# Kernel tuning notes

Measured on AMD Instinct MI355X. Metric: run time of the kernel, lower is better.

## Reference

```python
import jax, jax.numpy as jnp
import numpy as np

EPS_NORM = 1e-12


def _sage_layer(h, src, dst, n_dst, W_self, W_neigh, b):
    # DGL SAGEConv(mean) on a bipartite block: dst nodes = first n_dst src nodes.
    h_dst = h[:n_dst]
    msgs = h[src]                                              # [E, d] irregular gather
    s = jax.ops.segment_sum(msgs, dst, num_segments=n_dst)    # [n_dst, d]
    cnt = jax.ops.segment_sum(jnp.ones((src.shape[0],), h.dtype), dst, num_segments=n_dst)
    agg = s / jnp.maximum(cnt, 1.0)[:, None]                   # mean over in-neighbors (0-deg -> 0)
    out = h_dst @ W_self + agg @ W_neigh + b
    out = jax.nn.relu(out)                                     # activation=F.relu
    nrm = jnp.maximum(jnp.linalg.norm(out, axis=1, keepdims=True), EPS_NORM)
    return out / nrm                                           # norm=F.normalize


def setup_inputs() -> dict:
    key = jax.random.key(0)
    ks = jax.random.split(key, 16)
    N0, N1, N2 = 200000, 50000, 10000
    E0, E1 = 800000, 160000
    F_IN, H, L = 128, 256, 32
    x = jax.random.uniform(ks[0], (N0, F_IN), dtype=jnp.float32)
    src0 = jax.random.randint(ks[1], (E0,), 0, N0, dtype=jnp.int32)
    dst0 = jax.random.randint(ks[2], (E0,), 0, N1, dtype=jnp.int32)
    src1 = jax.random.randint(ks[3], (E1,), 0, N1, dtype=jnp.int32)
    dst1 = jax.random.randint(ks[4], (E1,), 0, N2, dtype=jnp.int32)
    sc = 0.05
    return {
        "x": x,
        "W_self0": jax.random.normal(ks[5], (F_IN, H), jnp.float32) * sc,
        "W_neigh0": jax.random.normal(ks[6], (F_IN, H), jnp.float32) * sc,
        "b0": jnp.zeros((H,), jnp.float32),
        "W_self1": jax.random.normal(ks[7], (H, H), jnp.float32) * sc,
        "W_neigh1": jax.random.normal(ks[8], (H, H), jnp.float32) * sc,
        "b1": jnp.zeros((H,), jnp.float32),
        "W_mu": jax.random.normal(ks[9], (H, L), jnp.float32) * sc,
        "b_mu": jnp.zeros((L,), jnp.float32),
        "W_var": jax.random.normal(ks[10], (H, L), jnp.float32) * sc,
        "b_var": jnp.zeros((L,), jnp.float32),
        "src0": src0, "dst0": dst0, "src1": src1, "dst1": dst1,
        "n_dst0": N1, "n_dst1": N2,
    }


def reference(x, W_self0, W_neigh0, b0, W_self1, W_neigh1, b1,
              W_mu, b_mu, W_var, b_var,
              src0, dst0, src1, dst1, n_dst0, n_dst1):
    h = jnp.log(x + 1.0)
    h = _sage_layer(h, src0, dst0, n_dst0, W_self0, W_neigh0, b0)
    h = _sage_layer(h, src1, dst1, n_dst1, W_self1, W_neigh1, b1)
    z_loc = h @ W_mu + b_mu
    z_scale = jnp.exp(h @ W_var + b_var) + 1e-6
    return (z_loc, z_scale)
```

## Files before the change

### kernel.cpp

```cpp
#include <hip/hip_runtime.h>
#include <math.h>

#define DEVI static __device__ __forceinline__

typedef __attribute__((ext_vector_type(8))) short s16x8;
typedef __attribute__((ext_vector_type(4))) float f32x4;

constexpr int CH = 4096;

DEVI float bf2f(unsigned short u) {
  union { unsigned int i; float f; } v; v.i = ((unsigned int)u) << 16; return v.f;
}
DEVI unsigned short f2bf(float f) {
  union { float f; unsigned int i; } v; v.f = f;
  return (unsigned short)((v.i + 0x7fffu + ((v.i >> 16) & 1u)) >> 16);
}

DEVI float fast_log1p(float x) {
  float t = x + 1.0f;
  float l;
  asm("v_log_f32 %0, %1" : "=v"(l) : "v"(t));
  return l * 0.6931471805599453f;
}

DEVI void log1p_span(const float* __restrict__ x, unsigned short* __restrict__ h0,
                     int lo, int hi, int blk, int nblk) {
  int stride = nblk * 256;
  for (int i = lo + blk * 256 + threadIdx.x; i < hi; i += stride) {
    float4 v = ((const float4*)x)[i];
    ushort4 o;
    o.x = f2bf(fast_log1p(v.x)); o.y = f2bf(fast_log1p(v.y));
    o.z = f2bf(fast_log1p(v.z)); o.w = f2bf(fast_log1p(v.w));
    ((ushort4*)h0)[i] = o;
  }
}

__global__ __launch_bounds__(256) void front_k(const int* __restrict__ dst0, int E0,
                                               const int* __restrict__ dst1, int E1,
                                               unsigned* __restrict__ gh, int B0, int B1,
                                               const float* __restrict__ Ws0, const float* __restrict__ Wn0,
                                               const float* __restrict__ Ws1, const float* __restrict__ Wn1,
                                               const float* __restrict__ Wmu, const float* __restrict__ Wvar,
                                               unsigned short* __restrict__ T0s, unsigned short* __restrict__ T0n,
                                               unsigned short* __restrict__ T1s, unsigned short* __restrict__ T1n,
                                               unsigned short* __restrict__ Thead) {
  __shared__ unsigned h[256];
  int b = blockIdx.x;
  int t = threadIdx.x;
  int BH = B0 + B1;
  if (b < BH) {
    bool L1 = b >= B0;
    const int* dst = L1 ? dst1 : dst0;
    int E = L1 ? E1 : E0;
    int base = L1 ? b - B0 : b;
    unsigned* out = L1 ? gh + 256 * B0 : gh;
    int B = L1 ? B1 : B0;
    h[t] = 0;
    __syncthreads();
    int e0 = base * CH, eend = min(e0 + CH, E);
    for (int i = e0 + t; i < eend; i += 256) atomicAdd(&h[((unsigned)dst[i]) >> 8], 1u);
    __syncthreads();
    out[t * B + base] = h[t];
  } else {
    int i = (b - BH) * 256 + t;
    if (i < 32768) {
      int hh = i >> 7, k = i & 127;
      T0s[i] = f2bf(Ws0[k * 256 + hh]);
      T0n[i] = f2bf(Wn0[k * 256 + hh]);
    }
    if (i < 65536) {
      int hh = i >> 8, k = i & 255;
      T1s[i] = f2bf(Ws1[k * 256 + hh]);
      T1n[i] = f2bf(Wn1[k * 256 + hh]);
    }
    if (i < 16384) {
      int c = i >> 8, k = i & 255;
      Thead[i] = f2bf(c < 32 ? Wmu[k * 32 + c] : Wvar[k * 32 + (c - 32)]);
    }
  }
}

__global__ void scan_block_sums_k(const unsigned* __restrict__ a, int M, unsigned* __restrict__ part) {
  __shared__ unsigned sm[256];
  int t = threadIdx.x;
  int i = blockIdx.x * 256 + t;
  sm[t] = (i < M) ? a[i] : 0u;
  __syncthreads();
  for (int o = 128; o > 0; o >>= 1) {
    if (t < o) sm[t] += sm[t + o];
    __syncthreads();
  }
  if (t == 0) part[blockIdx.x] = sm[0];
}

__global__ void scan_partials_k(unsigned* __restrict__ part, int P) {
  __shared__ unsigned sm[256];
  int t = threadIdx.x;
  unsigned v = (t < P) ? part[t] : 0u;
  sm[t] = v;
  __syncthreads();
  for (int o = 1; o < 256; o <<= 1) {
    unsigned xv = (t >= o) ? sm[t - o] : 0u;
    __syncthreads();
    sm[t] += xv;
    __syncthreads();
  }
  if (t < P) part[t] = sm[t] - v;
}

__global__ void scan_write_k(unsigned* __restrict__ a, int M, const unsigned* __restrict__ part) {
  __shared__ unsigned sm[256];
  int t = threadIdx.x;
  int i = blockIdx.x * 256 + t;
  unsigned v = (i < M) ? a[i] : 0u;
  sm[t] = v;
  __syncthreads();
  for (int o = 1; o < 256; o <<= 1) {
    unsigned xv = (t >= o) ? sm[t - o] : 0u;
    __syncthreads();
    sm[t] += xv;
    __syncthreads();
  }
  if (i < M) a[i] = part[blockIdx.x] + sm[t] - v;
}

__global__ __launch_bounds__(256) void scatter2_k(const int* __restrict__ src0, const int* __restrict__ dst0, int E0,
                                                  const int* __restrict__ src1, const int* __restrict__ dst1, int E1,
                                                  const unsigned* __restrict__ gh, int B0, int B1,
                                                  uint2* __restrict__ tmp,
                                                  const float* __restrict__ x, unsigned short* __restrict__ h0,
                                                  int n4h, int LS) {
  __shared__ unsigned cur[256];
  int b = blockIdx.x;
  int NB = B0 + B1;
  if (b >= NB) {
    log1p_span(x, h0, 0, n4h, b - NB, LS);
    return;
  }
  bool L1 = b >= B0;
  const int* dst = L1 ? dst1 : dst0;
  const int* src = L1 ? src1 : src0;
  int E = L1 ? E1 : E0;
  int base = L1 ? b - B0 : b;
  const unsigned* g = L1 ? gh + 256 * B0 : gh;
  int B = L1 ? B1 : B0;
  int t = threadIdx.x;
  cur[t] = g[t * B + base];
  __syncthreads();
  int e0 = base * CH, eend = min(e0 + CH, E);
  for (int i = e0 + t; i < eend; i += 256) {
    int d = dst[i];
    unsigned p = atomicAdd(&cur[((unsigned)d) >> 8], 1u);
    tmp[p] = make_uint2((unsigned)d, (unsigned)src[i]);
  }
}

__global__ __launch_bounds__(256) void finalize_k(const uint2* __restrict__ tmp, const unsigned* __restrict__ gh,
                                                  int B0, int B1, int N1, int N2,
                                                  unsigned* __restrict__ off, unsigned* __restrict__ cnt,
                                                  int* __restrict__ ss, int QB0, int QB1,
                                                  const float* __restrict__ x, unsigned short* __restrict__ h0,
                                                  int n4h, int n4, int LF) {
  __shared__ unsigned h[256];
  __shared__ unsigned sm[256];
  int q = blockIdx.x;
  int QF = QB0 + QB1;
  if (q >= QF) {
    log1p_span(x, h0, n4h, n4, q - QF, LF);
    return;
  }
  bool L1 = q >= QB0;
  int Nd = L1 ? N2 : N1;
  int qb = L1 ? q - QB0 : q;
  const unsigned* g = L1 ? gh + 256 * B0 : gh;
  int B = L1 ? B1 : B0;
  int t = threadIdx.x;
  unsigned bstart = g[qb * B];
  unsigned bend = g[(qb + 1) * B];
  unsigned nbk = bend - bstart;

  h[t] = 0;
  __syncthreads();
  for (unsigned i = t; i < nbk; i += 256) atomicAdd(&h[tmp[bstart + i].x & 255u], 1u);
  __syncthreads();
  unsigned v = h[t];
  sm[t] = v;
  __syncthreads();
  for (int o = 1; o < 256; o <<= 1) {
    unsigned xv = (t >= o) ? sm[t - o] : 0u;
    __syncthreads();
    sm[t] += xv;
    __syncthreads();
  }
  unsigned myoff = bstart + sm[t] - v;
  int dl = qb * 256 + t;
  if (dl < Nd) {
    int dg = (L1 ? N1 : 0) + dl;
    off[dg] = myoff;
    cnt[dg] = v;
  }
  __syncthreads();
  sm[t] = myoff;
  __syncthreads();
  for (unsigned i = t; i < nbk; i += 256) {
    uint2 e = tmp[bstart + i];
    unsigned p = atomicAdd(&sm[e.x & 255u], 1u);
    ss[p] = (int)e.y;
  }
}

template <int F>
__global__ __launch_bounds__(256) void aggregate_k(const unsigned short* __restrict__ hsrc,
                                                   const int* __restrict__ ss,
                                                   const unsigned* __restrict__ off,
                                                   const unsigned* __restrict__ cnt,
                                                   unsigned short* __restrict__ agg, int M) {
  constexpr int PL = F / 32;
  int w = threadIdx.x >> 6, l = threadIdx.x & 63;
  int half = l >> 5, c32 = l & 31;
  int d = blockIdx.x * 4 + w;
  if (d >= M) return;
  unsigned o = off[d];
  int n = (int)cnt[d];
  float fa[PL];
#pragma unroll
  for (int f = 0; f < PL; ++f) fa[f] = 0.f;

  int i = 0;
  for (; i + 16 <= n; i += 16) {
    int sv[8];
#pragma unroll
    for (int u = 0; u < 8; ++u) sv[u] = ss[o + i + 2 * u + half];
    if constexpr (PL == 4) {
      uint2 v[8];
#pragma unroll
      for (int u = 0; u < 8; ++u) v[u] = *(const uint2*)&hsrc[(size_t)sv[u] * F + c32 * 4];
#pragma unroll
      for (int u = 0; u < 8; ++u) {
        fa[0] += bf2f((unsigned short)(v[u].x & 0xffffu));
        fa[1] += bf2f((unsigned short)(v[u].x >> 16));
        fa[2] += bf2f((unsigned short)(v[u].y & 0xffffu));
        fa[3] += bf2f((unsigned short)(v[u].y >> 16));
      }
    } else {
      uint4 v[8];
#pragma unroll
      for (int u = 0; u < 8; ++u) v[u] = *(const uint4*)&hsrc[(size_t)sv[u] * F + c32 * 8];
#pragma unroll
      for (int u = 0; u < 8; ++u) {
        fa[0] += bf2f((unsigned short)(v[u].x & 0xffffu));
        fa[1] += bf2f((unsigned short)(v[u].x >> 16));
        fa[2] += bf2f((unsigned short)(v[u].y & 0xffffu));
        fa[3] += bf2f((unsigned short)(v[u].y >> 16));
        fa[4] += bf2f((unsigned short)(v[u].z & 0xffffu));
        fa[5] += bf2f((unsigned short)(v[u].z >> 16));
        fa[6] += bf2f((unsigned short)(v[u].w & 0xffffu));
        fa[7] += bf2f((unsigned short)(v[u].w >> 16));
      }
    }
  }
  for (; i < n; i += 2) {
    int e = i + half;
    bool val = e < n;
    int s = ss[o + (val ? e : i)];
    if constexpr (PL == 4) {
      uint2 v = *(const uint2*)&hsrc[(size_t)s * F + c32 * 4];
      unsigned vx = val ? v.x : 0u, vy = val ? v.y : 0u;
      fa[0] += bf2f((unsigned short)(vx & 0xffffu));
      fa[1] += bf2f((unsigned short)(vx >> 16));
      fa[2] += bf2f((unsigned short)(vy & 0xffffu));
      fa[3] += bf2f((unsigned short)(vy >> 16));
    } else {
      uint4 v = *(const uint4*)&hsrc[(size_t)s * F + c32 * 8];
      unsigned vx = val ? v.x : 0u, vy = val ? v.y : 0u;
      unsigned vz = val ? v.z : 0u, vw = val ? v.w : 0u;
      fa[0] += bf2f((unsigned short)(vx & 0xffffu));
      fa[1] += bf2f((unsigned short)(vx >> 16));
      fa[2] += bf2f((unsigned short)(vy & 0xffffu));
      fa[3] += bf2f((unsigned short)(vy >> 16));
      fa[4] += bf2f((unsigned short)(vz & 0xffffu));
      fa[5] += bf2f((unsigned short)(vz >> 16));
      fa[6] += bf2f((unsigned short)(vw & 0xffffu));
      fa[7] += bf2f((unsigned short)(vw >> 16));
    }
  }

#pragma unroll
  for (int f = 0; f < PL; ++f) fa[f] += __shfl_xor(fa[f], 32, 64);

  float inv = 1.0f / (float)((n > 0) ? n : 1);
  if (l < 32) {
    if constexpr (PL == 4) {
      uint2 ov;
      ov.x = (unsigned)f2bf(fa[0] * inv) | ((unsigned)f2bf(fa[1] * inv) << 16);
      ov.y = (unsigned)f2bf(fa[2] * inv) | ((unsigned)f2bf(fa[3] * inv) << 16);
      *(uint2*)&agg[(size_t)d * F + c32 * 4] = ov;
    } else {
      uint4 ov;
      ov.x = (unsigned)f2bf(fa[0] * inv) | ((unsigned)f2bf(fa[1] * inv) << 16);
      ov.y = (unsigned)f2bf(fa[2] * inv) | ((unsigned)f2bf(fa[3] * inv) << 16);
      ov.z = (unsigned)f2bf(fa[4] * inv) | ((unsigned)f2bf(fa[5] * inv) << 16);
      ov.w = (unsigned)f2bf(fa[6] * inv) | ((unsigned)f2bf(fa[7] * inv) << 16);
      *(uint4*)&agg[(size_t)d * F + c32 * 8] = ov;
    }
  }
}

template <int KD, bool HEAD>
__global__ __launch_bounds__(512) void layer_gemm_k(const unsigned short* __restrict__ Aself,
                                                    const unsigned short* __restrict__ Aagg,
                                                    const unsigned short* __restrict__ WtS,
                                                    const unsigned short* __restrict__ WtN,
                                                    const float* __restrict__ bias,
                                                    unsigned short* __restrict__ Hout,
                                                    const unsigned short* __restrict__ Thead,
                                                    const float* __restrict__ bmu, const float* __restrict__ bvar,
                                                    float* __restrict__ outp, int M) {
  __shared__ unsigned short At[128][40];
  __shared__ unsigned short Bt[256][40];
  __shared__ float rowsq[4][128];
  __shared__ float rowtot[128];
  __shared__ unsigned short h2t[HEAD ? 128 : 1][HEAD ? 264 : 1];

  int tid = threadIdx.x;
  int w = tid >> 6, l = tid & 63;
  int wr = w >> 2, wc = w & 3;
  int m0 = blockIdx.x * 128;

  f32x4 acc[4][4];
#pragma unroll
  for (int rt = 0; rt < 4; ++rt)
#pragma unroll
    for (int ct = 0; ct < 4; ++ct) acc[rt][ct] = (f32x4)(0.f);

  for (int s = 0; s < 2; ++s) {
    const unsigned short* A = s ? Aagg : Aself;
    const unsigned short* Wt = s ? WtN : WtS;
    for (int k0 = 0; k0 < KD; k0 += 32) {
      {
        int r = tid >> 2, c8 = (tid & 3) << 3;
        int gr = m0 + r;
        uint4 v = make_uint4(0, 0, 0, 0);
        if (gr < M) v = *(const uint4*)&A[(size_t)gr * KD + k0 + c8];
        *(uint4*)&At[r][c8] = v;
      }
#pragma unroll
      for (int rr = 0; rr < 2; ++rr) {
        int r = (tid >> 2) + (rr << 7), c8 = (tid & 3) << 3;
        uint4 v = *(const uint4*)&Wt[(size_t)r * KD + k0 + c8];
        *(uint4*)&Bt[r][c8] = v;
      }
      __syncthreads();
      s16x8 a[4], b[4];
#pragma unroll
      for (int rt = 0; rt < 4; ++rt) a[rt] = *(const s16x8*)&At[wr * 64 + rt * 16 + (l & 15)][(l >> 4) * 8];
#pragma unroll
      for (int ct = 0; ct < 4; ++ct) b[ct] = *(const s16x8*)&Bt[wc * 64 + ct * 16 + (l & 15)][(l >> 4) * 8];
#pragma unroll
      for (int rt = 0; rt < 4; ++rt)
#pragma unroll
        for (int ct = 0; ct < 4; ++ct)
          acc[rt][ct] = __builtin_amdgcn_mfma_f32_16x16x32_bf16(a[rt], b[ct], acc[rt][ct], 0, 0, 0);
      __syncthreads();
    }
  }

  float pr[4][4];
#pragma unroll
  for (int rt = 0; rt < 4; ++rt)
#pragma unroll
    for (int j = 0; j < 4; ++j) pr[rt][j] = 0.f;
#pragma unroll
  for (int rt = 0; rt < 4; ++rt)
#pragma unroll
    for (int ct = 0; ct < 4; ++ct) {
      int c = wc * 64 + ct * 16 + (l & 15);
      float bv = bias[c];
#pragma unroll
      for (int j = 0; j < 4; ++j) {
        float vv = acc[rt][ct][j] + bv;
        vv = fmaxf(vv, 0.f);
        acc[rt][ct][j] = vv;
        pr[rt][j] += vv * vv;
      }
    }
#pragma unroll
  for (int rt = 0; rt < 4; ++rt)
#pragma unroll
    for (int j = 0; j < 4; ++j) {
      float p = pr[rt][j];
      for (int m = 1; m < 16; m <<= 1) p += __shfl_xor(p, m, 64);
      pr[rt][j] = p;
    }
  if ((l & 15) == 0) {
#pragma unroll
    for (int rt = 0; rt < 4; ++rt)
#pragma unroll
      for (int j = 0; j < 4; ++j) rowsq[wc][wr * 64 + rt * 16 + (l >> 4) * 4 + j] = pr[rt][j];
  }
  __syncthreads();
  if (tid < 128) rowtot[tid] = rowsq[0][tid] + rowsq[1][tid] + rowsq[2][tid] + rowsq[3][tid];
  __syncthreads();

  if constexpr (!HEAD) {
#pragma unroll
    for (int rt = 0; rt < 4; ++rt) {
      int rbase = wr * 64 + rt * 16 + (l >> 4) * 4;
#pragma unroll
      for (int j = 0; j < 4; ++j) {
        int r = rbase + j;
        int gr = m0 + r;
        if (gr < M) {
          float inv = 1.0f / fmaxf(sqrtf(rowtot[r]), 1e-12f);
#pragma unroll
          for (int ct = 0; ct < 4; ++ct) {
            int c = wc * 64 + ct * 16 + (l & 15);
            Hout[(size_t)gr * 256 + c] = f2bf(acc[rt][ct][j] * inv);
          }
        }
      }
    }
  } else {
#pragma unroll
    for (int rt = 0; rt < 4; ++rt) {
      int rbase = wr * 64 + rt * 16 + (l >> 4) * 4;
#pragma unroll
      for (int j = 0; j < 4; ++j) {
        int r = rbase + j;
        float inv = 1.0f / fmaxf(sqrtf(rowtot[r]), 1e-12f);
#pragma unroll
        for (int ct = 0; ct < 4; ++ct) {
          int c = wc * 64 + ct * 16 + (l & 15);
          h2t[r][c] = f2bf(acc[rt][ct][j] * inv);
        }
      }
    }
    __syncthreads();

    const int arow = wr * 64 + (l & 15);
    const int kk = (l >> 4) * 8;
    f32x4 hacc[4];
#pragma unroll
    for (int rt = 0; rt < 4; ++rt) hacc[rt] = (f32x4)(0.f);
#pragma unroll
    for (int k0 = 0; k0 < 256; k0 += 32) {
      s16x8 ha[4];
#pragma unroll
      for (int rt = 0; rt < 4; ++rt) ha[rt] = *(const s16x8*)&h2t[arow + rt * 16][k0 + kk];
      s16x8 hb = *(const s16x8*)&Thead[(size_t)(wc * 16 + (l & 15)) * 256 + k0 + kk];
#pragma unroll
      for (int rt = 0; rt < 4; ++rt)
        hacc[rt] = __builtin_amdgcn_mfma_f32_16x16x32_bf16(ha[rt], hb, hacc[rt], 0, 0, 0);
    }
    const int c = wc * 16 + (l & 15);
    const float hbias = (c < 32) ? bmu[c] : bvar[c - 32];
#pragma unroll
    for (int rt = 0; rt < 4; ++rt)
#pragma unroll
      for (int j = 0; j < 4; ++j) {
        int gr = m0 + wr * 64 + rt * 16 + (l >> 4) * 4 + j;
        if (gr < M) {
          float val = hacc[rt][j] + hbias;
          if (c < 32)
            outp[(size_t)gr * 32 + c] = val;
          else
            outp[(size_t)M * 32 + (size_t)gr * 32 + (c - 32)] = expf(val) + 1e-6f;
        }
      }
  }
}

extern "C" void kernel_launch(void* const* d_in, const int* in_sizes, int n_in,
                              void* d_out, int out_size, void* d_ws, size_t ws_size,
                              hipStream_t stream) {
  const float* x    = (const float*)d_in[0];
  const float* Ws0  = (const float*)d_in[1];
  const float* Wn0  = (const float*)d_in[2];
  const float* b0   = (const float*)d_in[3];
  const float* Ws1  = (const float*)d_in[4];
  const float* Wn1  = (const float*)d_in[5];
  const float* b1   = (const float*)d_in[6];
  const float* Wmu  = (const float*)d_in[7];
  const float* bmu  = (const float*)d_in[8];
  const float* Wvar = (const float*)d_in[9];
  const float* bvar = (const float*)d_in[10];
  const int* src0   = (const int*)d_in[11];
  const int* dst0   = (const int*)d_in[12];
  const int* src1   = (const int*)d_in[13];
  const int* dst1   = (const int*)d_in[14];

  const int N0 = in_sizes[0] / 128;
  const int E0 = in_sizes[11];
  const int E1 = in_sizes[13];
  const int N1 = 50000, N2 = 10000;
  const int M = N1 + N2;

  char* ws = (char*)d_ws;
  size_t o = 0;
  auto take = [&](size_t b) -> char* {
    size_t cur = (o + 255) & ~(size_t)255;
    o = cur + b;
    return ws + cur;
  };
  unsigned short* h0    = (unsigned short*)take((size_t)N0 * 128 * 2);
  unsigned short* agg0  = (unsigned short*)take((size_t)N1 * 128 * 2);
  unsigned short* h1    = (unsigned short*)take((size_t)N1 * 256 * 2);
  unsigned short* agg1  = (unsigned short*)take((size_t)N2 * 256 * 2);
  unsigned short* T0s   = (unsigned short*)take(256 * 128 * 2);
  unsigned short* T0n   = (unsigned short*)take(256 * 128 * 2);
  unsigned short* T1s   = (unsigned short*)take(256 * 256 * 2);
  unsigned short* T1n   = (unsigned short*)take(256 * 256 * 2);
  unsigned short* Thead = (unsigned short*)take(64 * 256 * 2);

  int B0 = (E0 + CH - 1) / CH;
  int B1 = (E1 + CH - 1) / CH;
  int NB = B0 + B1;
  int G  = 256 * NB;
  int QB0 = (N1 + 255) / 256;
  int QB1 = (N2 + 255) / 256;
  int QF  = QB0 + QB1;

  unsigned* gh   = (unsigned*)take((size_t)G * 4);
  unsigned* off  = (unsigned*)take((size_t)M * 4);
  unsigned* cnt  = (unsigned*)take((size_t)M * 4);
  unsigned* part = (unsigned*)take(256 * 4);
  uint2* tmp = (uint2*)take((size_t)(E0 + E1) * 8);
  int* ss = (int*)take((size_t)(E0 + E1) * 4);
  (void)ws_size;

  const int n4 = N0 * 128 / 4;
  const int n4h = n4 / 2;
  const int LS = 1536, LF = 1536;

  front_k<<<NB + 256, 256, 0, stream>>>(dst0, E0, dst1, E1, gh, B0, B1,
                                        Ws0, Wn0, Ws1, Wn1, Wmu, Wvar,
                                        T0s, T0n, T1s, T1n, Thead);

  scan_block_sums_k<<<NB, 256, 0, stream>>>(gh, G, part);
  scan_partials_k<<<1, 256, 0, stream>>>(part, NB);
  scan_write_k<<<NB, 256, 0, stream>>>(gh, G, part);

  scatter2_k<<<NB + LS, 256, 0, stream>>>(src0, dst0, E0, src1, dst1, E1, gh, B0, B1, tmp,
                                          x, h0, n4h, LS);
  finalize_k<<<QF + LF, 256, 0, stream>>>(tmp, gh, B0, B1, N1, N2, off, cnt, ss, QB0, QB1,
                                          x, h0, n4h, n4, LF);

  aggregate_k<128><<<(N1 + 3) / 4, 256, 0, stream>>>(h0, ss, off, cnt, agg0, N1);
  layer_gemm_k<128, false><<<(N1 + 127) / 128, 512, 0, stream>>>(h0, agg0, T0s, T0n, b0,
                                                                 h1, nullptr, nullptr, nullptr, nullptr, N1);

  aggregate_k<256><<<(N2 + 3) / 4, 256, 0, stream>>>(h1, ss, off + N1, cnt + N1, agg1, N2);
  layer_gemm_k<256, true><<<(N2 + 127) / 128, 512, 0, stream>>>(h1, agg1, T1s, T1n, b1,
                                                                nullptr, Thead, bmu, bvar, (float*)d_out, N2);
}
```

Measured before the change: 168.0 us.

## Spread log1p work across preprocessing kernels and merge scan partials step

The log1p conversion of x is now split into five spans and piggybacked onto the histogram, scan-sum, scan-write, scatter and finalize kernels, so the bandwidth-bound conversion overlaps the small latency-bound CSR-build kernels. The separate scan_partials kernel is removed: each scan_write block recomputes the prefix over the block partials itself, which drops one launch. The aggregate tail also gains 8- and 4-edge unrolled steps before the scalar remainder. This adds extra blocks to every preprocessing kernel, and the split ratios are hand-tuned.

```diff
diff --git a/kernel.cpp b/kernel.cpp
--- a/kernel.cpp
+++ b/kernel.cpp
@@ -43,7 +43,9 @@
                                                const float* __restrict__ Wmu, const float* __restrict__ Wvar,
                                                unsigned short* __restrict__ T0s, unsigned short* __restrict__ T0n,
                                                unsigned short* __restrict__ T1s, unsigned short* __restrict__ T1n,
-                                               unsigned short* __restrict__ Thead) {
+                                               unsigned short* __restrict__ Thead,
+                                               const float* __restrict__ x, unsigned short* __restrict__ h0,
+                                               int lo, int hi, int LA) {
   __shared__ unsigned h[256];
   int b = blockIdx.x;
   int t = threadIdx.x;
@@ -61,7 +63,7 @@
     for (int i = e0 + t; i < eend; i += 256) atomicAdd(&h[((unsigned)dst[i]) >> 8], 1u);
     __syncthreads();
     out[t * B + base] = h[t];
-  } else {
+  } else if (b < BH + 256) {
     int i = (b - BH) * 256 + t;
     if (i < 32768) {
       int hh = i >> 7, k = i & 127;
@@ -77,27 +79,36 @@
       int c = i >> 8, k = i & 255;
       Thead[i] = f2bf(c < 32 ? Wmu[k * 32 + c] : Wvar[k * 32 + (c - 32)]);
     }
-  }
-}
-
-__global__ void scan_block_sums_k(const unsigned* __restrict__ a, int M, unsigned* __restrict__ part) {
+  } else {
+    log1p_span(x, h0, lo, hi, b - BH - 256, LA);
+  }
+}
+
+__global__ __launch_bounds__(256) void scan_sums_k(const unsigned* __restrict__ a, int NB,
+                                                   unsigned* __restrict__ part,
+                                                   const float* __restrict__ x, unsigned short* __restrict__ h0,
+                                                   int lo, int hi, int LB) {
   __shared__ unsigned sm[256];
-  int t = threadIdx.x;
-  int i = blockIdx.x * 256 + t;
-  sm[t] = (i < M) ? a[i] : 0u;
+  int b = blockIdx.x, t = threadIdx.x;
+  if (b >= NB) { log1p_span(x, h0, lo, hi, b - NB, LB); return; }
+  sm[t] = a[b * 256 + t];
   __syncthreads();
   for (int o = 128; o > 0; o >>= 1) {
     if (t < o) sm[t] += sm[t + o];
     __syncthreads();
   }
-  if (t == 0) part[blockIdx.x] = sm[0];
-}
-
-__global__ void scan_partials_k(unsigned* __restrict__ part, int P) {
+  if (t == 0) part[b] = sm[0];
+}
+
+__global__ __launch_bounds__(256) void scan_write_k(unsigned* __restrict__ a, int NB,
+                                                    const unsigned* __restrict__ part,
+                                                    const float* __restrict__ x, unsigned short* __restrict__ h0,
+                                                    int lo, int hi, int LC) {
   __shared__ unsigned sm[256];
-  int t = threadIdx.x;
-  unsigned v = (t < P) ? part[t] : 0u;
-  sm[t] = v;
+  int b = blockIdx.x, t = threadIdx.x;
+  if (b >= NB) { log1p_span(x, h0, lo, hi, b - NB, LC); return; }
+  unsigned pv = (t < NB) ? part[t] : 0u;
+  sm[t] = pv;
   __syncthreads();
   for (int o = 1; o < 256; o <<= 1) {
     unsigned xv = (t >= o) ? sm[t - o] : 0u;
@@ -105,14 +116,9 @@
     sm[t] += xv;
     __syncthreads();
   }
-  if (t < P) part[t] = sm[t] - v;
-}
-
-__global__ void scan_write_k(unsigned* __restrict__ a, int M, const unsigned* __restrict__ part) {
-  __shared__ unsigned sm[256];
-  int t = threadIdx.x;
-  int i = blockIdx.x * 256 + t;
-  unsigned v = (i < M) ? a[i] : 0u;
+  unsigned pb = (b == 0) ? 0u : sm[b - 1];
+  __syncthreads();
+  unsigned v = a[b * 256 + t];
   sm[t] = v;
   __syncthreads();
   for (int o = 1; o < 256; o <<= 1) {
@@ -121,7 +127,7 @@
     sm[t] += xv;
     __syncthreads();
   }
-  if (i < M) a[i] = part[blockIdx.x] + sm[t] - v;
+  a[b * 256 + t] = pb + sm[t] - v;
 }
 
 __global__ __launch_bounds__(256) void scatter2_k(const int* __restrict__ src0, const int* __restrict__ dst0, int E0,
@@ -129,14 +135,11 @@
                                                   const unsigned* __restrict__ gh, int B0, int B1,
                                                   uint2* __restrict__ tmp,
                                                   const float* __restrict__ x, unsigned short* __restrict__ h0,
-                                                  int n4h, int LS) {
+                                                  int lo, int hi, int LS) {
   __shared__ unsigned cur[256];
   int b = blockIdx.x;
   int NB = B0 + B1;
-  if (b >= NB) {
-    log1p_span(x, h0, 0, n4h, b - NB, LS);
-    return;
-  }
+  if (b >= NB) { log1p_span(x, h0, lo, hi, b - NB, LS); return; }
   bool L1 = b >= B0;
   const int* dst = L1 ? dst1 : dst0;
   const int* src = L1 ? src1 : src0;
@@ -160,15 +163,12 @@
                                                   unsigned* __restrict__ off, unsigned* __restrict__ cnt,
                                                   int* __restrict__ ss, int QB0, int QB1,
                                                   const float* __restrict__ x, unsigned short* __restrict__ h0,
-                                                  int n4h, int n4, int LF) {
+                                                  int lo, int hi, int LF) {
   __shared__ unsigned h[256];
   __shared__ unsigned sm[256];
   int q = blockIdx.x;
   int QF = QB0 + QB1;
-  if (q >= QF) {
-    log1p_span(x, h0, n4h, n4, q - QF, LF);
-    return;
-  }
+  if (q >= QF) { log1p_span(x, h0, lo, hi, q - QF, LF); return; }
   bool L1 = q >= QB0;
   int Nd = L1 ? N2 : N1;
   int qb = L1 ? q - QB0 : q;
@@ -206,6 +206,42 @@
     uint2 e = tmp[bstart + i];
     unsigned p = atomicAdd(&sm[e.x & 255u], 1u);
     ss[p] = (int)e.y;
+  }
+}
+
+template <int UL, int PL>
+DEVI void gstep(const unsigned short* __restrict__ hsrc, const int* __restrict__ ss,
+                unsigned base, int half, int c32, float* fa) {
+  constexpr int F = PL * 32;
+  int sv[UL];
+#pragma unroll
+  for (int u = 0; u < UL; ++u) sv[u] = ss[base + 2 * u + half];
+  if constexpr (PL == 4) {
+    uint2 v[UL];
+#pragma unroll
+    for (int u = 0; u < UL; ++u) v[u] = *(const uint2*)&hsrc[(size_t)sv[u] * F + c32 * 4];
+#pragma unroll
+    for (int u = 0; u < UL; ++u) {
+      fa[0] += bf2f((unsigned short)(v[u].x & 0xffffu));
+      fa[1] += bf2f((unsigned short)(v[u].x >> 16));
+      fa[2] += bf2f((unsigned short)(v[u].y & 0xffffu));
+      fa[3] += bf2f((unsigned short)(v[u].y >> 16));
+    }
+  } else {
+    uint4 v[UL];
+#pragma unroll
+    for (int u = 0; u < UL; ++u) v[u] = *(const uint4*)&hsrc[(size_t)sv[u] * F + c32 * 8];
+#pragma unroll
+    for (int u = 0; u < UL; ++u) {
+      fa[0] += bf2f((unsigned short)(v[u].x & 0xffffu));
+      fa[1] += bf2f((unsigned short)(v[u].x >> 16));
+      fa[2] += bf2f((unsigned short)(v[u].y & 0xffffu));
+      fa[3] += bf2f((unsigned short)(v[u].y >> 16));
+      fa[4] += bf2f((unsigned short)(v[u].z & 0xffffu));
+      fa[5] += bf2f((unsigned short)(v[u].z >> 16));
+      fa[6] += bf2f((unsigned short)(v[u].w & 0xffffu));
+      fa[7] += bf2f((unsigned short)(v[u].w >> 16));
+    }
   }
 }
 
@@ -227,38 +263,9 @@
   for (int f = 0; f < PL; ++f) fa[f] = 0.f;
 
   int i = 0;
-  for (; i + 16 <= n; i += 16) {
-    int sv[8];
-#pragma unroll
-    for (int u = 0; u < 8; ++u) sv[u] = ss[o + i + 2 * u + half];
-    if constexpr (PL == 4) {
-      uint2 v[8];
-#pragma unroll
-      for (int u = 0; u < 8; ++u) v[u] = *(const uint2*)&hsrc[(size_t)sv[u] * F + c32 * 4];
-#pragma unroll
-      for (int u = 0; u < 8; ++u) {
-        fa[0] += bf2f((unsigned short)(v[u].x & 0xffffu));
-        fa[1] += bf2f((unsigned short)(v[u].x >> 16));
-        fa[2] += bf2f((unsigned short)(v[u].y & 0xffffu));
-        fa[3] += bf2f((unsigned short)(v[u].y >> 16));
-      }
-    } else {
-      uint4 v[8];
-#pragma unroll
-      for (int u = 0; u < 8; ++u) v[u] = *(const uint4*)&hsrc[(size_t)sv[u] * F + c32 * 8];
-#pragma unroll
-      for (int u = 0; u < 8; ++u) {
-        fa[0] += bf2f((unsigned short)(v[u].x & 0xffffu));
-        fa[1] += bf2f((unsigned short)(v[u].x >> 16));
-        fa[2] += bf2f((unsigned short)(v[u].y & 0xffffu));
-        fa[3] += bf2f((unsigned short)(v[u].y >> 16));
-        fa[4] += bf2f((unsigned short)(v[u].z & 0xffffu));
-        fa[5] += bf2f((unsigned short)(v[u].z >> 16));
-        fa[6] += bf2f((unsigned short)(v[u].w & 0xffffu));
-        fa[7] += bf2f((unsigned short)(v[u].w >> 16));
-      }
-    }
-  }
+  for (; i + 16 <= n; i += 16) gstep<8, PL>(hsrc, ss, o + i, half, c32, fa);
+  if (i + 8 <= n) { gstep<4, PL>(hsrc, ss, o + i, half, c32, fa); i += 8; }
+  if (i + 4 <= n) { gstep<2, PL>(hsrc, ss, o + i, half, c32, fa); i += 4; }
   for (; i < n; i += 2) {
     int e = i + half;
     bool val = e < n;
@@ -529,21 +536,21 @@
   (void)ws_size;
 
   const int n4 = N0 * 128 / 4;
-  const int n4h = n4 / 2;
-  const int LS = 1536, LF = 1536;
-
-  front_k<<<NB + 256, 256, 0, stream>>>(dst0, E0, dst1, E1, gh, B0, B1,
-                                        Ws0, Wn0, Ws1, Wn1, Wmu, Wvar,
-                                        T0s, T0n, T1s, T1n, Thead);
-
-  scan_block_sums_k<<<NB, 256, 0, stream>>>(gh, G, part);
-  scan_partials_k<<<1, 256, 0, stream>>>(part, NB);
-  scan_write_k<<<NB, 256, 0, stream>>>(gh, G, part);
+  const int c1 = n4 * 8 / 100, c2 = n4 * 16 / 100, c3 = n4 * 25 / 100, c4 = n4 * 60 / 100;
+  const int LA = 768, LBs = 768, LC = 768, LS = 1536, LF = 1536;
+
+  front_k<<<NB + 256 + LA, 256, 0, stream>>>(dst0, E0, dst1, E1, gh, B0, B1,
+                                             Ws0, Wn0, Ws1, Wn1, Wmu, Wvar,
+                                             T0s, T0n, T1s, T1n, Thead,
+                                             x, h0, 0, c1, LA);
+
+  scan_sums_k<<<NB + LBs, 256, 0, stream>>>(gh, NB, part, x, h0, c1, c2, LBs);
+  scan_write_k<<<NB + LC, 256, 0, stream>>>(gh, NB, part, x, h0, c2, c3, LC);
 
   scatter2_k<<<NB + LS, 256, 0, stream>>>(src0, dst0, E0, src1, dst1, E1, gh, B0, B1, tmp,
-                                          x, h0, n4h, LS);
+                                          x, h0, c3, c4, LS);
   finalize_k<<<QF + LF, 256, 0, stream>>>(tmp, gh, B0, B1, N1, N2, off, cnt, ss, QB0, QB1,
-                                          x, h0, n4h, n4, LF);
+                                          x, h0, c4, n4, LF);
 
   aggregate_k<128><<<(N1 + 3) / 4, 256, 0, stream>>>(h0, ss, off, cnt, agg0, N1);
   layer_gemm_k<128, false><<<(N1 + 127) / 128, 512, 0, stream>>>(h0, agg0, T0s, T0n, b0,
```

Measured after the change: 157.4 us. -6.3%, faster.
